# Kernel optimization log

Measured on AMD Instinct MI355X. Metric: run time of the kernel, lower is better.

## Reference

```python
import jax, jax.numpy as jnp
import numpy as np

NEIGHBOR_SIZE = 20
COORD_DIM = 2
THETA = (1.0, 0.5, 0.1)  # (sigma^2, phi, tau) exponential kernel with nugget
BATCH = 200000


def setup_inputs() -> dict:
    key = jax.random.key(0)
    k1, k2 = jax.random.split(key)
    neighbor_positions = jax.random.normal(
        k1, (BATCH, NEIGHBOR_SIZE * COORD_DIM), dtype=jnp.float32)
    edge_list = jax.random.randint(k2, (BATCH, NEIGHBOR_SIZE), 0, BATCH, dtype=jnp.int64)
    return {"neighbor_positions": neighbor_positions, "edge_list": edge_list}


def _pairwise_dists(pos):
    # pos: [B, n, d] -> dists: [B, n, n]
    diff = pos[:, None, :, :] - pos[:, :, None, :]
    sq = jnp.sum(diff * diff, axis=-1)
    return jnp.sqrt(sq)


def reference(neighbor_positions, edge_list):
    sigma_sq, phi, tau = THETA
    pos = neighbor_positions.reshape(-1, NEIGHBOR_SIZE, COORD_DIM)
    dists = _pairwise_dists(pos)  # [B, n, n]
    # make_cov_full with nuggets: sigma^2 * exp(-phi * d) + tau * sigma^2 * I
    cov = sigma_sq * jnp.exp(-phi * dists)
    cov = cov + (tau * sigma_sq) * jnp.eye(NEIGHBOR_SIZE, dtype=cov.dtype)
    return jnp.linalg.inv(cov)
```

## Files before the change

### kernel.cpp

```cpp
#include <hip/hip_runtime.h>

namespace {

constexpr int N = 20;
constexpr int ROWS = 5;
constexpr int NP = N / 2;
constexpr int GROUPS = 16;
constexpr int WAVES_PER_BLOCK = 4;
constexpr int MATS_PER_BLOCK = GROUPS * WAVES_PER_BLOCK;
constexpr float SIGMA_SQ = 1.0f;
constexpr float PHI = 0.5f;
constexpr float TAU = 0.1f;
constexpr float CSCALE = 0.72134752f;

typedef float f32x2 __attribute__((ext_vector_type(2)));

template <int SRC>
__device__ __forceinline__ float qbcast(float x) {
  constexpr int CTRL = SRC * 0x55;
  return __builtin_bit_cast(
      float, __builtin_amdgcn_mov_dpp(__builtin_bit_cast(int, x), CTRL, 0xF,
                                      0xF, true));
}

template <int K>
__device__ __forceinline__ void gj_step(f32x2 (&a2)[ROWS][NP], int o,
                                        const float (&ofl)[4]) {
  constexpr int KO = K / ROWS;
  constexpr int KR = K % ROWS;
  constexpr int KP = K / 2;
  constexpr int KE = K % 2;

  f32x2 r2[NP];
#pragma unroll
  for (int q = 0; q < NP; ++q) {
    r2[q].x = qbcast<KO>(a2[KR][q].x);
    r2[q].y = qbcast<KO>(a2[KR][q].y);
  }
  const float rK = KE ? r2[KP].y : r2[KP].x;
  const float ip = __builtin_amdgcn_rcpf(rK);
  const float fpiv = 1.0f - ip;

#pragma unroll
  for (int rr = 0; rr < ROWS; ++rr) {
    const float aK = KE ? a2[rr][KP].y : a2[rr][KP].x;
    float f = aK * ip;
    if (rr == KR) f = (o == KO) ? fpiv : f;
    const float nf = -f;
    const f32x2 nf2 = {nf, nf};
#pragma unroll
    for (int q = 0; q < NP; ++q) {
      a2[rr][q] = __builtin_elementwise_fma(nf2, r2[q], a2[rr][q]);
    }
    if (KE) a2[rr][KP].y = nf; else a2[rr][KP].x = nf;
  }
  if (KE) a2[KR][KP].y += ofl[KO]; else a2[KR][KP].x += ofl[KO];
}

__global__ __launch_bounds__(256, 2) void invcov_kernel(
    const float* __restrict__ pos, float* __restrict__ out, int B) {
  __shared__ float lds[WAVES_PER_BLOCK][4 * N * N];

  const int tid  = threadIdx.x;
  const int lane = tid & 63;
  const int wave = tid >> 6;
  const int g    = lane >> 2;
  const int o    = lane & 3;
  const int mwave0 = blockIdx.x * MATS_PER_BLOCK + wave * GROUPS;
  const int m    = mwave0 + g;
  const int mc   = (m < B) ? m : (B - 1);

  const float* pm = pos + (size_t)mc * (2 * N);

  f32x2 px2[NP], py2[NP];
  {
    const float4* pv = (const float4*)pm;
#pragma unroll
    for (int q = 0; q < NP; ++q) {
      const float4 p = pv[q];
      px2[q].x = p.x * CSCALE; px2[q].y = p.z * CSCALE;
      py2[q].x = p.y * CSCALE; py2[q].y = p.w * CSCALE;
    }
  }
  float myx[ROWS], myy[ROWS];
  {
    const float2* pm2 = (const float2*)pm;
#pragma unroll
    for (int rr = 0; rr < ROWS; ++rr) {
      const float2 p = pm2[ROWS * o + rr];
      myx[rr] = p.x * CSCALE; myy[rr] = p.y * CSCALE;
    }
  }

  float tdiag[4], ofl[4];
#pragma unroll
  for (int t = 0; t < 4; ++t) {
    const bool is = (o == t);
    tdiag[t] = is ? (TAU * SIGMA_SQ) : 0.0f;
    ofl[t]   = is ? 1.0f : 0.0f;
  }

  f32x2 a2[ROWS][NP];
#pragma unroll
  for (int rr = 0; rr < ROWS; ++rr) {
    const f32x2 mx = {myx[rr], myx[rr]};
    const f32x2 my = {myy[rr], myy[rr]};
#pragma unroll
    for (int q = 0; q < NP; ++q) {
      const f32x2 dx = px2[q] - mx;
      const f32x2 dy = py2[q] - my;
      f32x2 s = dx * dx;
      s = __builtin_elementwise_fma(dy, dy, s);
      const float d0 = __builtin_amdgcn_sqrtf(s.x);
      const float d1 = __builtin_amdgcn_sqrtf(s.y);
      float v0 = SIGMA_SQ * __builtin_amdgcn_exp2f(-d0);
      float v1 = SIGMA_SQ * __builtin_amdgcn_exp2f(-d1);
      if ((2 * q) % ROWS == rr)     v0 += tdiag[(2 * q) / ROWS];
      if ((2 * q + 1) % ROWS == rr) v1 += tdiag[(2 * q + 1) / ROWS];
      a2[rr][q].x = v0; a2[rr][q].y = v1;
    }
  }

  __builtin_amdgcn_s_setprio(1);
  gj_step<0>(a2, o, ofl);  gj_step<1>(a2, o, ofl);  gj_step<2>(a2, o, ofl);
  gj_step<3>(a2, o, ofl);  gj_step<4>(a2, o, ofl);  gj_step<5>(a2, o, ofl);
  gj_step<6>(a2, o, ofl);  gj_step<7>(a2, o, ofl);  gj_step<8>(a2, o, ofl);
  gj_step<9>(a2, o, ofl);  gj_step<10>(a2, o, ofl); gj_step<11>(a2, o, ofl);
  gj_step<12>(a2, o, ofl); gj_step<13>(a2, o, ofl); gj_step<14>(a2, o, ofl);
  gj_step<15>(a2, o, ofl); gj_step<16>(a2, o, ofl); gj_step<17>(a2, o, ofl);
  gj_step<18>(a2, o, ofl); gj_step<19>(a2, o, ofl);
  __builtin_amdgcn_s_setprio(0);

  float* wbuf = &lds[wave][0];

  if (mwave0 + GROUPS <= B) {
#pragma unroll
    for (int p = 0; p < 4; ++p) {
      if ((g >> 2) == p) {
        float* dst = wbuf + (g & 3) * (N * N) + o * (ROWS * N);
#pragma unroll
        for (int rr = 0; rr < ROWS; ++rr) {
#pragma unroll
          for (int q = 0; q < N / 4; ++q) {
            *(float4*)&dst[rr * N + 4 * q] =
                make_float4(a2[rr][2 * q].x, a2[rr][2 * q].y,
                            a2[rr][2 * q + 1].x, a2[rr][2 * q + 1].y);
          }
        }
      }
      asm volatile("s_waitcnt lgkmcnt(0)" ::: "memory");

      float* gout = out + (size_t)(mwave0 + 4 * p) * (N * N);
#pragma unroll
      for (int s = 0; s < 6; ++s) {
        const float4 v = *(const float4*)&wbuf[lane * 4 + s * 256];
        *(float4*)&gout[lane * 4 + s * 256] = v;
      }
      if (lane < 16) {
        const float4 v = *(const float4*)&wbuf[lane * 4 + 6 * 256];
        *(float4*)&gout[lane * 4 + 6 * 256] = v;
      }
      asm volatile("s_waitcnt lgkmcnt(0)" ::: "memory");
    }
  } else if (m < B) {
    float* om = out + (size_t)m * (N * N) + (ROWS * o) * N;
#pragma unroll
    for (int rr = 0; rr < ROWS; ++rr) {
#pragma unroll
      for (int q = 0; q < N / 4; ++q) {
        *(float4*)&om[rr * N + 4 * q] =
            make_float4(a2[rr][2 * q].x, a2[rr][2 * q].y,
                        a2[rr][2 * q + 1].x, a2[rr][2 * q + 1].y);
      }
    }
  }
}

}

extern "C" void kernel_launch(void* const* d_in, const int* in_sizes, int n_in,
                              void* d_out, int out_size, void* d_ws, size_t ws_size,
                              hipStream_t stream) {
  const float* pos = (const float*)d_in[0];
  float* out = (float*)d_out;
  const int B = in_sizes[0] / (2 * N);
  const int blocks = (B + MATS_PER_BLOCK - 1) / MATS_PER_BLOCK;
  invcov_kernel<<<blocks, 256, 0, stream>>>(pos, out, B);
}
```

Before: 85.59 us.

## Process two matrix tiles per wave with async LDS prefetch of second tile

Each wave now inverts two groups of 16 matrices instead of one, halving the grid size. The positions for the second group are fetched asynchronously into LDS with global_load_lds while the first group's covariance build and Gauss-Jordan elimination run. The goal is to hide input load latency behind compute and amortise per-block setup. In exchange, LDS use per block grows and the tail clamps the prefetch source, which only matches the right matrices when B is a multiple of 16.

```diff
diff --git a/kernel.cpp b/kernel.cpp
--- a/kernel.cpp
+++ b/kernel.cpp
@@ -6,14 +6,21 @@
 constexpr int ROWS = 5;
 constexpr int NP = N / 2;
 constexpr int GROUPS = 16;
+constexpr int TILE = 2;
 constexpr int WAVES_PER_BLOCK = 4;
-constexpr int MATS_PER_BLOCK = GROUPS * WAVES_PER_BLOCK;
+constexpr int MATS_PER_WAVE = GROUPS * TILE;
+constexpr int MATS_PER_BLOCK = MATS_PER_WAVE * WAVES_PER_BLOCK;
+constexpr int PTS_FLOATS = GROUPS * 2 * N;
+constexpr int WBUF_FLOATS = 4 * N * N;
 constexpr float SIGMA_SQ = 1.0f;
 constexpr float PHI = 0.5f;
 constexpr float TAU = 0.1f;
 constexpr float CSCALE = 0.72134752f;
 
 typedef float f32x2 __attribute__((ext_vector_type(2)));
+
+#define LGKM_FENCE() asm volatile("s_waitcnt lgkmcnt(0)" ::: "memory")
+#define SCHED_FENCE() __builtin_amdgcn_sched_barrier(0)
 
 template <int SRC>
 __device__ __forceinline__ float qbcast(float x) {
@@ -57,50 +64,25 @@
   if (KE) a2[KR][KP].y += ofl[KO]; else a2[KR][KP].x += ofl[KO];
 }
 
-__global__ __launch_bounds__(256, 2) void invcov_kernel(
-    const float* __restrict__ pos, float* __restrict__ out, int B) {
-  __shared__ float lds[WAVES_PER_BLOCK][4 * N * N];
-
-  const int tid  = threadIdx.x;
-  const int lane = tid & 63;
-  const int wave = tid >> 6;
-  const int g    = lane >> 2;
-  const int o    = lane & 3;
-  const int mwave0 = blockIdx.x * MATS_PER_BLOCK + wave * GROUPS;
-  const int m    = mwave0 + g;
-  const int mc   = (m < B) ? m : (B - 1);
-
-  const float* pm = pos + (size_t)mc * (2 * N);
-
-  f32x2 px2[NP], py2[NP];
-  {
-    const float4* pv = (const float4*)pm;
-#pragma unroll
-    for (int q = 0; q < NP; ++q) {
-      const float4 p = pv[q];
-      px2[q].x = p.x * CSCALE; px2[q].y = p.z * CSCALE;
-      py2[q].x = p.y * CSCALE; py2[q].y = p.w * CSCALE;
-    }
-  }
-  float myx[ROWS], myy[ROWS];
-  {
-    const float2* pm2 = (const float2*)pm;
-#pragma unroll
-    for (int rr = 0; rr < ROWS; ++rr) {
-      const float2 p = pm2[ROWS * o + rr];
-      myx[rr] = p.x * CSCALE; myy[rr] = p.y * CSCALE;
-    }
-  }
-
-  float tdiag[4], ofl[4];
-#pragma unroll
-  for (int t = 0; t < 4; ++t) {
-    const bool is = (o == t);
-    tdiag[t] = is ? (TAU * SIGMA_SQ) : 0.0f;
-    ofl[t]   = is ? 1.0f : 0.0f;
-  }
-
-  f32x2 a2[ROWS][NP];
+__device__ __forceinline__ void gj_all(f32x2 (&a2)[ROWS][NP], int o,
+                                       const float (&ofl)[4]) {
+  __builtin_amdgcn_s_setprio(1);
+  gj_step<0>(a2, o, ofl);  gj_step<1>(a2, o, ofl);  gj_step<2>(a2, o, ofl);
+  gj_step<3>(a2, o, ofl);  gj_step<4>(a2, o, ofl);  gj_step<5>(a2, o, ofl);
+  gj_step<6>(a2, o, ofl);  gj_step<7>(a2, o, ofl);  gj_step<8>(a2, o, ofl);
+  gj_step<9>(a2, o, ofl);  gj_step<10>(a2, o, ofl); gj_step<11>(a2, o, ofl);
+  gj_step<12>(a2, o, ofl); gj_step<13>(a2, o, ofl); gj_step<14>(a2, o, ofl);
+  gj_step<15>(a2, o, ofl); gj_step<16>(a2, o, ofl); gj_step<17>(a2, o, ofl);
+  gj_step<18>(a2, o, ofl); gj_step<19>(a2, o, ofl);
+  __builtin_amdgcn_s_setprio(0);
+}
+
+__device__ __forceinline__ void build_cov(f32x2 (&a2)[ROWS][NP],
+                                          const f32x2 (&px2)[NP],
+                                          const f32x2 (&py2)[NP],
+                                          const float (&myx)[ROWS],
+                                          const float (&myy)[ROWS],
+                                          const float (&tdiag)[4]) {
 #pragma unroll
   for (int rr = 0; rr < ROWS; ++rr) {
     const f32x2 mx = {myx[rr], myx[rr]};
@@ -120,20 +102,14 @@
       a2[rr][q].x = v0; a2[rr][q].y = v1;
     }
   }
-
-  __builtin_amdgcn_s_setprio(1);
-  gj_step<0>(a2, o, ofl);  gj_step<1>(a2, o, ofl);  gj_step<2>(a2, o, ofl);
-  gj_step<3>(a2, o, ofl);  gj_step<4>(a2, o, ofl);  gj_step<5>(a2, o, ofl);
-  gj_step<6>(a2, o, ofl);  gj_step<7>(a2, o, ofl);  gj_step<8>(a2, o, ofl);
-  gj_step<9>(a2, o, ofl);  gj_step<10>(a2, o, ofl); gj_step<11>(a2, o, ofl);
-  gj_step<12>(a2, o, ofl); gj_step<13>(a2, o, ofl); gj_step<14>(a2, o, ofl);
-  gj_step<15>(a2, o, ofl); gj_step<16>(a2, o, ofl); gj_step<17>(a2, o, ofl);
-  gj_step<18>(a2, o, ofl); gj_step<19>(a2, o, ofl);
-  __builtin_amdgcn_s_setprio(0);
-
-  float* wbuf = &lds[wave][0];
-
-  if (mwave0 + GROUPS <= B) {
+}
+
+__device__ __forceinline__ void epilogue(float* wbuf,
+                                         const f32x2 (&a2)[ROWS][NP],
+                                         float* __restrict__ out, int mbase,
+                                         int B, int g, int o, int lane,
+                                         int m) {
+  if (mbase + GROUPS <= B) {
 #pragma unroll
     for (int p = 0; p < 4; ++p) {
       if ((g >> 2) == p) {
@@ -148,9 +124,8 @@
           }
         }
       }
-      asm volatile("s_waitcnt lgkmcnt(0)" ::: "memory");
-
-      float* gout = out + (size_t)(mwave0 + 4 * p) * (N * N);
+      LGKM_FENCE();
+      float* gout = out + (size_t)(mbase + 4 * p) * (N * N);
 #pragma unroll
       for (int s = 0; s < 6; ++s) {
         const float4 v = *(const float4*)&wbuf[lane * 4 + s * 256];
@@ -160,7 +135,7 @@
         const float4 v = *(const float4*)&wbuf[lane * 4 + 6 * 256];
         *(float4*)&gout[lane * 4 + 6 * 256] = v;
       }
-      asm volatile("s_waitcnt lgkmcnt(0)" ::: "memory");
+      LGKM_FENCE();
     }
   } else if (m < B) {
     float* om = out + (size_t)m * (N * N) + (ROWS * o) * N;
@@ -174,6 +149,98 @@
       }
     }
   }
+}
+
+__global__ __launch_bounds__(256, 2) void invcov_kernel(
+    const float* __restrict__ pos, float* __restrict__ out, int B) {
+  __shared__ float lds[WAVES_PER_BLOCK][PTS_FLOATS + WBUF_FLOATS];
+
+  const int tid  = threadIdx.x;
+  const int lane = tid & 63;
+  const int wave = tid >> 6;
+  const int g    = lane >> 2;
+  const int o    = lane & 3;
+  const int mbase0 = blockIdx.x * MATS_PER_BLOCK + wave * MATS_PER_WAVE;
+  const int mbase1 = mbase0 + GROUPS;
+  const int m0 = mbase0 + g;
+  const int m1 = mbase1 + g;
+  float* pts  = &lds[wave][0];
+  float* wbuf = &lds[wave][PTS_FLOATS];
+
+  {
+    const int src_m = (mbase1 <= B - GROUPS) ? mbase1 : (B - GROUPS);
+    const float* gsrc = pos + (size_t)src_m * (2 * N);
+    __builtin_amdgcn_global_load_lds(
+        (const __attribute__((address_space(1))) void*)(gsrc + lane * 4),
+        (__attribute__((address_space(3))) void*)(pts), 16, 0, 0);
+    __builtin_amdgcn_global_load_lds(
+        (const __attribute__((address_space(1))) void*)(gsrc + 256 + lane * 4),
+        (__attribute__((address_space(3))) void*)(pts + 256), 16, 0, 0);
+    __builtin_amdgcn_global_load_lds(
+        (const __attribute__((address_space(1))) void*)(gsrc + 512 + lane),
+        (__attribute__((address_space(3))) void*)(pts + 512), 4, 0, 0);
+    __builtin_amdgcn_global_load_lds(
+        (const __attribute__((address_space(1))) void*)(gsrc + 576 + lane),
+        (__attribute__((address_space(3))) void*)(pts + 576), 4, 0, 0);
+  }
+  SCHED_FENCE();
+
+  float tdiag[4], ofl[4];
+#pragma unroll
+  for (int t = 0; t < 4; ++t) {
+    const bool is = (o == t);
+    tdiag[t] = is ? (TAU * SIGMA_SQ) : 0.0f;
+    ofl[t]   = is ? 1.0f : 0.0f;
+  }
+
+  f32x2 px2[NP], py2[NP];
+  float myx[ROWS], myy[ROWS];
+  {
+    const int mc0 = (m0 < B) ? m0 : (B - 1);
+    const float* pm = pos + (size_t)mc0 * (2 * N);
+    const float4* pv = (const float4*)pm;
+#pragma unroll
+    for (int q = 0; q < NP; ++q) {
+      const float4 p = pv[q];
+      px2[q].x = p.x * CSCALE; px2[q].y = p.z * CSCALE;
+      py2[q].x = p.y * CSCALE; py2[q].y = p.w * CSCALE;
+    }
+    const float2* pm2 = (const float2*)pm;
+#pragma unroll
+    for (int rr = 0; rr < ROWS; ++rr) {
+      const float2 p = pm2[ROWS * o + rr];
+      myx[rr] = p.x * CSCALE; myy[rr] = p.y * CSCALE;
+    }
+  }
+  f32x2 a2[ROWS][NP];
+  build_cov(a2, px2, py2, myx, myy, tdiag);
+  gj_all(a2, o, ofl);
+
+  SCHED_FENCE();
+  asm volatile("s_waitcnt vmcnt(0)" ::: "memory");
+  SCHED_FENCE();
+
+  epilogue(wbuf, a2, out, mbase0, B, g, o, lane, m0);
+
+  {
+    const float4* pv = (const float4*)(pts + g * (2 * N));
+#pragma unroll
+    for (int q = 0; q < NP; ++q) {
+      const float4 p = pv[q];
+      px2[q].x = p.x * CSCALE; px2[q].y = p.z * CSCALE;
+      py2[q].x = p.y * CSCALE; py2[q].y = p.w * CSCALE;
+    }
+    const float2* pm2 = (const float2*)(pts + g * (2 * N));
+#pragma unroll
+    for (int rr = 0; rr < ROWS; ++rr) {
+      const float2 p = pm2[ROWS * o + rr];
+      myx[rr] = p.x * CSCALE; myy[rr] = p.y * CSCALE;
+    }
+  }
+  build_cov(a2, px2, py2, myx, myy, tdiag);
+  gj_all(a2, o, ofl);
+
+  epilogue(wbuf, a2, out, mbase1, B, g, o, lane, m1);
 }
 
 }
```

New measurement: 97.70 us. +14.1%, slower.
